# Optimization experiments

Measured on AMD Instinct MI355X. Metric: run time of the kernel, lower is better.

## Reference

```python
import jax, jax.numpy as jnp
import numpy as np

RADIUS = 0.1
MAX_GRID_DIM = 96
MAX_COLLISIONS = 128


def setup_inputs() -> dict:
    key = jax.random.key(0)
    k1, k2 = jax.random.split(key)
    locs = jax.random.uniform(k1, (2, 4096, 3), dtype=jnp.float32)
    data = jax.random.normal(k2, (2, 4096, 16), dtype=jnp.float32)
    return {"locs": locs, "data": data}


def _cell_ids(locs):
    # Reproduces the grid-bound math in ParticleCollision.forward.
    lower = locs.min(axis=1)   # [B,D]
    upper = locs.max(axis=1)   # [B,D]
    grid_dims = jnp.ceil(jnp.clip((upper - lower) / RADIUS, 0.0, MAX_GRID_DIM))
    center = (lower + upper) * 0.5
    lower = center - grid_dims * RADIUS * 0.5
    gd = jnp.maximum(grid_dims, 1.0)
    cells = jnp.floor((locs - lower[:, None, :]) / RADIUS)
    cells = jnp.clip(cells, 0.0, gd[:, None, :] - 1.0).astype(jnp.int32)
    gdi = gd.astype(jnp.int32)  # [B,D]
    # Row-major strides per batch: stride[d] = prod(gdi[d+1:])
    rev_cp = jnp.cumprod(gdi[:, ::-1], axis=1)[:, ::-1]  # [B,D]
    strides = jnp.concatenate(
        [rev_cp[:, 1:], jnp.ones((gdi.shape[0], 1), jnp.int32)], axis=1)
    return (cells * strides[:, None, :]).sum(-1)  # [B,N]


def reference(locs, data):
    B, N, D = locs.shape
    cell_ids = _cell_ids(locs)
    # Stable sort by cell id (mirrors the radix sort); idxs = original index
    # of each particle in the new (sorted) order.
    order = jnp.argsort(cell_ids, axis=1, stable=True)  # [B,N]
    locs_s = jnp.take_along_axis(locs, order[:, :, None], axis=1)  # reordered locs
    data_s = jnp.take_along_axis(data, order[:, :, None], axis=1)  # reordered data
    # Pairwise squared distances without materializing [B,N,N,D].
    sq = (locs_s * locs_s).sum(-1)  # [B,N]
    d2 = sq[:, :, None] + sq[:, None, :] - 2.0 * jnp.einsum(
        'bnd,bmd->bnm', locs_s, locs_s)  # [B,N,N]
    mask = d2 <= RADIUS * RADIUS
    # First MAX_COLLISIONS in-radius neighbors per particle (ascending index
    # in sorted order), -1 padding past the end of each neighbor list.
    keys = jnp.where(mask, jnp.int32(0), jnp.int32(1))
    nbr = jnp.argsort(keys, axis=-1, stable=True)[:, :, :MAX_COLLISIONS]
    valid = jnp.take_along_axis(mask, nbr, axis=-1)
    neighbors = jnp.where(valid, nbr, -1).astype(jnp.float32)  # [B,N,M]
    idxs = order.astype(jnp.float32)  # [B,N]
    return idxs, neighbors, locs_s, data_s
```

## Files before the change

kernel.cpp:

```cpp
#include <hip/hip_runtime.h>

#define NPART 4096
#define NBATCH 2
#define MAXC 128

__global__ __launch_bounds__(256) void rank_kernel(
    const float* __restrict__ locs, unsigned short* __restrict__ partial,
    int njlog2, int jspan) {
  const int bx = blockIdx.x;
  const int tid = threadIdx.x;
  const int jslice = bx & ((1 << njlog2) - 1);
  const int ic = (bx >> njlog2) & 15;
  const int b = bx >> (njlog2 + 4);

  __shared__ float smn[3][256];
  __shared__ float smx[3][256];
  __shared__ int scj[256];
  __shared__ float sb_lower[3];
  __shared__ int sb_gdi[3];

  const float* base = locs + (size_t)b * NPART * 3;
  float mn0 = 1e30f, mn1 = 1e30f, mn2 = 1e30f;
  float mx0 = -1e30f, mx1 = -1e30f, mx2 = -1e30f;
  for (int n = tid; n < NPART; n += 256) {
    float x = base[n * 3 + 0];
    float y = base[n * 3 + 1];
    float z = base[n * 3 + 2];
    mn0 = fminf(mn0, x); mx0 = fmaxf(mx0, x);
    mn1 = fminf(mn1, y); mx1 = fmaxf(mx1, y);
    mn2 = fminf(mn2, z); mx2 = fmaxf(mx2, z);
  }
  smn[0][tid] = mn0; smn[1][tid] = mn1; smn[2][tid] = mn2;
  smx[0][tid] = mx0; smx[1][tid] = mx1; smx[2][tid] = mx2;
  __syncthreads();
  for (int s = 128; s > 0; s >>= 1) {
    if (tid < s) {
      for (int d = 0; d < 3; d++) {
        smn[d][tid] = fminf(smn[d][tid], smn[d][tid + s]);
        smx[d][tid] = fmaxf(smx[d][tid], smx[d][tid + s]);
      }
    }
    __syncthreads();
  }
  if (tid == 0) {
    for (int d = 0; d < 3; d++) {
      float lo = smn[d][0];
      float up = smx[d][0];
      float t = (up - lo) / 0.1f;
      t = fminf(fmaxf(t, 0.0f), 96.0f);
      float gdim = ceilf(t);
      float ctr = (lo + up) * 0.5f;
      float l2 = ctr - ((gdim * 0.1f) * 0.5f);
      float g = fmaxf(gdim, 1.0f);
      sb_lower[d] = l2;
      sb_gdi[d] = (int)g;
    }
  }
  __syncthreads();

  auto cid = [&](int n) {
    int c[3];
    for (int d = 0; d < 3; d++) {
      float v = base[n * 3 + d];
      float cf = floorf((v - sb_lower[d]) / 0.1f);
      float gdf = (float)sb_gdi[d];
      cf = fminf(fmaxf(cf, 0.0f), gdf - 1.0f);
      c[d] = (int)cf;
    }
    return (c[0] * sb_gdi[1] + c[1]) * sb_gdi[2] + c[2];
  };

  const int ci = cid(ic * 256 + tid);
  int cnt = 0;
  for (int jj = 0; jj < jspan; jj++) {
    int jc = jslice * jspan + jj;
    __syncthreads();
    scj[tid] = cid(jc * 256 + tid);
    __syncthreads();
    if (jc < ic) {
#pragma unroll 8
      for (int j = 0; j < 256; j++) cnt += (scj[j] <= ci);
    } else if (jc > ic) {
#pragma unroll 8
      for (int j = 0; j < 256; j++) cnt += (scj[j] < ci);
    } else {
#pragma unroll 8
      for (int j = 0; j < 256; j++) {
        int cj = scj[j];
        cnt += (cj < ci) || (cj == ci && j < tid);
      }
    }
  }
  partial[(size_t)jslice * (NBATCH * NPART) + b * NPART + ic * 256 + tid] =
      (unsigned short)cnt;
}

__global__ __launch_bounds__(256) void scatgather_kernel(
    const float* __restrict__ locs, const float* __restrict__ data,
    const unsigned short* __restrict__ partial, int nj,
    float* __restrict__ out_idxs, float* __restrict__ out_locs,
    float* __restrict__ out_data, float4* __restrict__ slocs) {
  int p = blockIdx.x * 256 + threadIdx.x;
  int pb = p >> 12;
  int i = p & (NPART - 1);
  int r = 0;
  for (int s = 0; s < nj; s++)
    r += (int)partial[(size_t)s * (NBATCH * NPART) + p];
  const float* src = locs + (size_t)p * 3;
  float x = src[0], y = src[1], z = src[2];
  float sq = __fadd_rn(__fadd_rn(__fmul_rn(x, x), __fmul_rn(y, y)),
                       __fmul_rn(z, z));
  size_t dst = (size_t)pb * NPART + r;
  out_idxs[dst] = (float)i;
  out_locs[dst * 3 + 0] = x;
  out_locs[dst * 3 + 1] = y;
  out_locs[dst * 3 + 2] = z;
  slocs[dst] = make_float4(x, y, z, sq);
  const float4* dsrc = (const float4*)(data + (size_t)p * 16);
  float4* ddst = (float4*)(out_data + dst * 16);
  for (int k = 0; k < 4; k++) ddst[k] = dsrc[k];
}

__global__ __launch_bounds__(256) void nbr_kernel(
    const float4* __restrict__ slocs, float* __restrict__ out_nbr) {
  const int b = blockIdx.y;
  __shared__ float4 sl[2048];
  const int tid = threadIdx.x;
  const int wave = tid >> 6, lane = tid & 63;
  const int row0 = blockIdx.x * 8 + wave * 2;
  const float4* sb = slocs + (size_t)b * NPART;
  const float4 me0 = sb[row0 + 0];
  const float4 me1 = sb[row0 + 1];
  float* r0 = out_nbr + ((size_t)b * NPART + row0) * MAXC;
  float* r1 = r0 + MAXC;
  int c0 = 0, c1 = 0;
  const unsigned long long lmask = (1ull << lane) - 1ull;
  for (int half = 0; half < 2; half++) {
    const int hbase = half * 2048;
    __syncthreads();
    for (int k = 0; k < 8; k++) {
      int j = k * 256 + tid;
      __builtin_amdgcn_global_load_lds(
          (const __attribute__((address_space(1))) unsigned int*)(sb + hbase +
                                                                  j),
          (__attribute__((address_space(3))) unsigned int*)&sl[j], 16, 0, 0);
    }
    __syncthreads();
#pragma unroll 4
    for (int base = 0; base < 2048; base += 64) {
      float4 o = sl[base + lane];
      float fm = (float)(hbase + base + lane);
#define DO_ROW(ME, CN, RP)                                                  \
      {                                                                     \
        float dot = __fmaf_rn(ME.z, o.z,                                    \
                     __fmaf_rn(ME.y, o.y, __fmul_rn(ME.x, o.x)));           \
        float d2 = __fsub_rn(__fadd_rn(ME.w, o.w), __fmul_rn(2.0f, dot));   \
        bool hit = d2 <= 0.01f;                                             \
        unsigned long long bal = __ballot(hit);                             \
        int pos = CN + __popcll(bal & lmask);                               \
        if (hit && pos < MAXC) RP[pos] = fm;                                \
        CN += __popcll(bal);                                                \
      }
      DO_ROW(me0, c0, r0)
      DO_ROW(me1, c1, r1)
#undef DO_ROW
    }
  }
  for (int q = min(c0, MAXC) + lane; q < MAXC; q += 64) r0[q] = -1.0f;
  for (int q = min(c1, MAXC) + lane; q < MAXC; q += 64) r1[q] = -1.0f;
}

extern "C" void kernel_launch(void* const* d_in, const int* in_sizes, int n_in,
                              void* d_out, int out_size, void* d_ws,
                              size_t ws_size, hipStream_t stream) {
  const float* locs = (const float*)d_in[0];
  const float* data = (const float*)d_in[1];

  float* out = (float*)d_out;
  float* out_idxs = out;
  float* out_nbr = out + NBATCH * NPART;
  float* out_locs = out_nbr + (size_t)NBATCH * NPART * MAXC;
  float* out_data = out_locs + (size_t)NBATCH * NPART * 3;

  float4* slocs = (float4*)d_ws;
  unsigned short* partial =
      (unsigned short*)((char*)d_ws + (size_t)NBATCH * NPART * 16);

  size_t base_bytes = (size_t)NBATCH * NPART * 16;
  int nj, njlog2;
  if (ws_size >= base_bytes + 16ull * NBATCH * NPART * 2) {
    nj = 16; njlog2 = 4;
  } else {
    nj = 4; njlog2 = 2;
  }
  int jspan = 16 / nj;

  rank_kernel<<<NBATCH * 16 * nj, 256, 0, stream>>>(locs, partial, njlog2,
                                                    jspan);
  scatgather_kernel<<<NBATCH * NPART / 256, 256, 0, stream>>>(
      locs, data, partial, nj, out_idxs, out_locs, out_data, slocs);
  nbr_kernel<<<dim3(NPART / 8, NBATCH), 256, 0, stream>>>(slocs, out_nbr);
}
```

Baseline: 89.90 us.

## Fuse rank computation and scatter into one kernel with per-block full cell-id table

Merges the rank-counting and scatter/gather kernels into a single launch. Each of 512 blocks recomputes all 4096 cell ids into shared memory, then 16 lanes per particle split the comparison range and reduce with shuffles, removing the partial-count buffer and one kernel launch. The cost is redundant min/max reduction and cell-id computation in every block, plus a 16 KB shared table per block.

```diff
diff --git a/kernel.cpp b/kernel.cpp
--- a/kernel.cpp
+++ b/kernel.cpp
@@ -4,22 +4,23 @@
 #define NBATCH 2
 #define MAXC 128
 
-__global__ __launch_bounds__(256) void rank_kernel(
-    const float* __restrict__ locs, unsigned short* __restrict__ partial,
-    int njlog2, int jspan) {
+__global__ __launch_bounds__(256) void rank_scat_kernel(
+    const float* __restrict__ locs, const float* __restrict__ data,
+    float* __restrict__ out_idxs, float* __restrict__ out_locs,
+    float* __restrict__ out_data, float4* __restrict__ slocs) {
   const int bx = blockIdx.x;
   const int tid = threadIdx.x;
-  const int jslice = bx & ((1 << njlog2) - 1);
-  const int ic = (bx >> njlog2) & 15;
-  const int b = bx >> (njlog2 + 4);
+  const int b = bx >> 8;
+  const int g = bx & 255;
 
   __shared__ float smn[3][256];
   __shared__ float smx[3][256];
-  __shared__ int scj[256];
+  __shared__ int scj[NPART];
   __shared__ float sb_lower[3];
   __shared__ int sb_gdi[3];
 
   const float* base = locs + (size_t)b * NPART * 3;
+
   float mn0 = 1e30f, mn1 = 1e30f, mn2 = 1e30f;
   float mx0 = -1e30f, mx1 = -1e30f, mx2 = -1e30f;
   for (int n = tid; n < NPART; n += 256) {
@@ -51,14 +52,15 @@
       float gdim = ceilf(t);
       float ctr = (lo + up) * 0.5f;
       float l2 = ctr - ((gdim * 0.1f) * 0.5f);
-      float g = fmaxf(gdim, 1.0f);
+      float g2 = fmaxf(gdim, 1.0f);
       sb_lower[d] = l2;
-      sb_gdi[d] = (int)g;
+      sb_gdi[d] = (int)g2;
     }
   }
   __syncthreads();
 
-  auto cid = [&](int n) {
+  for (int k = 0; k < 16; k++) {
+    int n = tid + k * 256;
     int c[3];
     for (int d = 0; d < 3; d++) {
       float v = base[n * 3 + d];
@@ -67,58 +69,43 @@
       cf = fminf(fmaxf(cf, 0.0f), gdf - 1.0f);
       c[d] = (int)cf;
     }
-    return (c[0] * sb_gdi[1] + c[1]) * sb_gdi[2] + c[2];
-  };
+    scj[n] = (c[0] * sb_gdi[1] + c[1]) * sb_gdi[2] + c[2];
+  }
+  __syncthreads();
 
-  const int ci = cid(ic * 256 + tid);
+  const int lane = tid & 63;
+  const int il = tid >> 4;
+  const int q = tid & 15;
+  const int i = g * 16 + il;
+  const int ci = scj[i];
   int cnt = 0;
-  for (int jj = 0; jj < jspan; jj++) {
-    int jc = jslice * jspan + jj;
-    __syncthreads();
-    scj[tid] = cid(jc * 256 + tid);
-    __syncthreads();
-    if (jc < ic) {
+  const int jb = q * 256;
 #pragma unroll 8
-      for (int j = 0; j < 256; j++) cnt += (scj[j] <= ci);
-    } else if (jc > ic) {
-#pragma unroll 8
-      for (int j = 0; j < 256; j++) cnt += (scj[j] < ci);
-    } else {
-#pragma unroll 8
-      for (int j = 0; j < 256; j++) {
-        int cj = scj[j];
-        cnt += (cj < ci) || (cj == ci && j < tid);
-      }
-    }
+  for (int it = 0; it < 256; it++) {
+    int j = jb + ((it + q) & 255);
+    int cj = scj[j];
+    cnt += (cj < ci) || (cj == ci && j < i);
   }
-  partial[(size_t)jslice * (NBATCH * NPART) + b * NPART + ic * 256 + tid] =
-      (unsigned short)cnt;
-}
+  cnt += __shfl_down(cnt, 8);
+  cnt += __shfl_down(cnt, 4);
+  cnt += __shfl_down(cnt, 2);
+  cnt += __shfl_down(cnt, 1);
+  const int r = __shfl(cnt, lane & ~15);
 
-__global__ __launch_bounds__(256) void scatgather_kernel(
-    const float* __restrict__ locs, const float* __restrict__ data,
-    const unsigned short* __restrict__ partial, int nj,
-    float* __restrict__ out_idxs, float* __restrict__ out_locs,
-    float* __restrict__ out_data, float4* __restrict__ slocs) {
-  int p = blockIdx.x * 256 + threadIdx.x;
-  int pb = p >> 12;
-  int i = p & (NPART - 1);
-  int r = 0;
-  for (int s = 0; s < nj; s++)
-    r += (int)partial[(size_t)s * (NBATCH * NPART) + p];
-  const float* src = locs + (size_t)p * 3;
-  float x = src[0], y = src[1], z = src[2];
-  float sq = __fadd_rn(__fadd_rn(__fmul_rn(x, x), __fmul_rn(y, y)),
-                       __fmul_rn(z, z));
-  size_t dst = (size_t)pb * NPART + r;
-  out_idxs[dst] = (float)i;
-  out_locs[dst * 3 + 0] = x;
-  out_locs[dst * 3 + 1] = y;
-  out_locs[dst * 3 + 2] = z;
-  slocs[dst] = make_float4(x, y, z, sq);
-  const float4* dsrc = (const float4*)(data + (size_t)p * 16);
-  float4* ddst = (float4*)(out_data + dst * 16);
-  for (int k = 0; k < 4; k++) ddst[k] = dsrc[k];
+  const size_t dst = (size_t)b * NPART + r;
+  if (q == 0) {
+    float x = base[i * 3 + 0];
+    float y = base[i * 3 + 1];
+    float z = base[i * 3 + 2];
+    float sq = __fadd_rn(__fadd_rn(__fmul_rn(x, x), __fmul_rn(y, y)),
+                         __fmul_rn(z, z));
+    out_idxs[dst] = (float)i;
+    out_locs[dst * 3 + 0] = x;
+    out_locs[dst * 3 + 1] = y;
+    out_locs[dst * 3 + 2] = z;
+    slocs[dst] = make_float4(x, y, z, sq);
+  }
+  out_data[dst * 16 + q] = data[((size_t)b * NPART + i) * 16 + q];
 }
 
 __global__ __launch_bounds__(256) void nbr_kernel(
@@ -166,8 +153,8 @@
 #undef DO_ROW
     }
   }
-  for (int q = min(c0, MAXC) + lane; q < MAXC; q += 64) r0[q] = -1.0f;
-  for (int q = min(c1, MAXC) + lane; q < MAXC; q += 64) r1[q] = -1.0f;
+  for (int p = min(c0, MAXC) + lane; p < MAXC; p += 64) r0[p] = -1.0f;
+  for (int p = min(c1, MAXC) + lane; p < MAXC; p += 64) r1[p] = -1.0f;
 }
 
 extern "C" void kernel_launch(void* const* d_in, const int* in_sizes, int n_in,
@@ -183,21 +170,8 @@
   float* out_data = out_locs + (size_t)NBATCH * NPART * 3;
 
   float4* slocs = (float4*)d_ws;
-  unsigned short* partial =
-      (unsigned short*)((char*)d_ws + (size_t)NBATCH * NPART * 16);
 
-  size_t base_bytes = (size_t)NBATCH * NPART * 16;
-  int nj, njlog2;
-  if (ws_size >= base_bytes + 16ull * NBATCH * NPART * 2) {
-    nj = 16; njlog2 = 4;
-  } else {
-    nj = 4; njlog2 = 2;
-  }
-  int jspan = 16 / nj;
-
-  rank_kernel<<<NBATCH * 16 * nj, 256, 0, stream>>>(locs, partial, njlog2,
-                                                    jspan);
-  scatgather_kernel<<<NBATCH * NPART / 256, 256, 0, stream>>>(
-      locs, data, partial, nj, out_idxs, out_locs, out_data, slocs);
+  rank_scat_kernel<<<NBATCH * 256, 256, 0, stream>>>(
+      locs, data, out_idxs, out_locs, out_data, slocs);
   nbr_kernel<<<dim3(NPART / 8, NBATCH), 256, 0, stream>>>(slocs, out_nbr);
 }
```

Result: slower. 103.6 us (+15.3%).
